# Optimization experiments

Measured on AMD Instinct MI355X. Metric: run time of the kernel, lower is better.

## Reference

```python
import jax, jax.numpy as jnp
import numpy as np

B, L, E, D = 4, 1024, 128, 256
NPOI, EPOI, NH, FF = 10000, 128, 8, 256
HD = D // NH


def layer_norm(x, g, b, eps=1e-5):
    m = x.mean(-1, keepdims=True)
    v = ((x - m) ** 2).mean(-1, keepdims=True)
    return (x - m) / jnp.sqrt(v + eps) * g + b


def leaky_relu(x):
    return jnp.where(x >= 0, x, 0.01 * x)


def tokenize_timestamp(t):
    # t: (..., 2) = [timestamp_sec, delta_sec] -> (..., 4) = [week, hour, minute, d_minute]
    week = t[..., 0] % 604800.0 / 86400.0
    hour = t[..., 0] % 86400.0 / 3600.0
    minute = t[..., 0] % 3600.0 / 60.0
    return jnp.stack([week, hour, minute, t[..., 1] / 60.0], -1)


def pos_encode(pos, d):
    # standard sinusoidal PE evaluated at integer positions `pos`
    freq = jnp.exp(-jnp.log(10000.0) * (2.0 * jnp.arange(d // 2, dtype=jnp.float32)) / d)
    ang = pos[..., None].astype(jnp.float32) * freq  # (..., d/2)
    pe = jnp.zeros(pos.shape + (d,), jnp.float32)
    return pe.at[..., 0::2].set(jnp.sin(ang)).at[..., 1::2].set(jnp.cos(ang))


def setup_inputs():
    ks = iter(jax.random.split(jax.random.key(0), 48))

    def nrm(shape, s=0.02):
        return jax.random.normal(next(ks), shape, jnp.float32) * s

    spatial = jax.random.normal(next(ks), (B, L, 2), jnp.float32) * 10.0
    ts = jax.random.uniform(next(ks), (B, L), jnp.float32, 0.0, 1e6)
    dt = jax.random.uniform(next(ks), (B, L), jnp.float32, 0.0, 3600.0)
    token = jax.random.randint(next(ks), (B, L, 2), 0, 2).astype(jnp.float32)
    iq = jnp.zeros((B, L, 4, 2), jnp.float32)
    iq = iq.at[..., 0, 0].set(spatial[..., 0]).at[..., 1, 0].set(spatial[..., 1])
    iq = iq.at[..., 2, 0].set(ts).at[..., 3, 0].set(dt)
    iq = iq.at[..., 0, 1].set(token[..., 0]).at[..., 2, 1].set(token[..., 1])
    positions = jax.random.randint(next(ks), (B, L, 2), 0, L)
    return dict(
        input_seq=iq, positions=positions,
        poi_coors=jax.random.normal(next(ks), (NPOI, 2), jnp.float32) * 10.0,
        poi_embed_mat=nrm((NPOI, EPOI), 1.0),
        sp_w1=nrm((2, E)), sp_b1=jnp.zeros((E,), jnp.float32),
        sp_w2=nrm((E, D)), sp_b2=jnp.zeros((D,), jnp.float32),
        four_w=nrm((4, E), 1.0), four_b=nrm((4, E), 1.0),
        te_w=nrm((4 * E, D)), te_b=jnp.zeros((D,), jnp.float32),
        poi_ln_g=jnp.ones((EPOI,), jnp.float32), poi_ln_b=jnp.zeros((EPOI,), jnp.float32),
        poi_w=nrm((EPOI, D)), poi_b=jnp.zeros((D,), jnp.float32),
        tok_emb=nrm((6, E), 1.0).at[5].set(0.0),
        tok_ln_g=jnp.ones((E,), jnp.float32), tok_ln_b=jnp.zeros((E,), jnp.float32),
        tok_w=nrm((E, D)), tok_b=jnp.zeros((D,), jnp.float32),
        mha_in_w=nrm((D, 3 * D)), mha_in_b=jnp.zeros((3 * D,), jnp.float32),
        mha_out_w=nrm((D, D)), mha_out_b=jnp.zeros((D,), jnp.float32),
        ln1_g=jnp.ones((D,), jnp.float32), ln1_b=jnp.zeros((D,), jnp.float32),
        ff_w1=nrm((D, FF)), ff_b1=jnp.zeros((FF,), jnp.float32),
        ff_w2=nrm((FF, D)), ff_b2=jnp.zeros((D,), jnp.float32),
        ln2_g=jnp.ones((D,), jnp.float32), ln2_b=jnp.zeros((D,), jnp.float32))


def reference(input_seq, positions, poi_coors, poi_embed_mat,
              sp_w1, sp_b1, sp_w2, sp_b2, four_w, four_b, te_w, te_b,
              poi_ln_g, poi_ln_b, poi_w, poi_b,
              tok_emb, tok_ln_g, tok_ln_b, tok_w, tok_b,
              mha_in_w, mha_in_b, mha_out_w, mha_out_b,
              ln1_g, ln1_b, ff_w1, ff_b1, ff_w2, ff_b2, ln2_g, ln2_b):
    token = input_seq[..., jnp.array([0, 2]), 1].astype(jnp.int32)  # (B,L,2)
    spatial = input_seq[:, :, 0:2, 0]                                # (B,L,2)
    tt = tokenize_timestamp(input_seq[:, :, 2:4, 0])                 # (B,L,4)
    # token embedding: Embedding(6) -> LN -> Linear -> (B,L,2,D)
    tok_e = layer_norm(tok_emb[token], tok_ln_g, tok_ln_b) @ tok_w + tok_b
    # spatial embedding (note: original's masked_fill is non-inplace and discarded)
    sp_e = leaky_relu(spatial @ sp_w1 + sp_b1) @ sp_w2 + sp_b2 + tok_e[:, :, 0]
    # brute-force nearest POI: cdist^2 + argmin + gather
    d2 = ((poi_coors[None, None] - spatial[:, :, None]) ** 2).sum(-1)  # (B,L,NPOI)
    poi = jnp.argmin(d2, -1)                                           # (B,L)
    poi_e = layer_norm(poi_embed_mat[poi], poi_ln_g, poi_ln_b) @ poi_w + poi_b + tok_e[:, :, 0]
    # temporal: 4 FourierEncode modules -> concat -> LeakyReLU -> Linear
    t_e = jnp.cos(tt[..., None] * four_w + four_b).reshape(B, L, 4 * E)
    t_e = leaky_relu(t_e) @ te_w + te_b + tok_e[:, :, 1]
    # modal mixer: 1-layer post-norm TransformerEncoder over the 3 modalities
    x = jnp.stack([sp_e, t_e, poi_e], 2).reshape(B * L, 3, D)
    qkv = x @ mha_in_w + mha_in_b
    q, k, v = jnp.split(qkv, 3, -1)
    q = q.reshape(B * L, 3, NH, HD)
    k = k.reshape(B * L, 3, NH, HD)
    v = v.reshape(B * L, 3, NH, HD)
    att = jax.nn.softmax(jnp.einsum('nqhd,nkhd->nhqk', q, k) / jnp.sqrt(jnp.float32(HD)), -1)
    o = jnp.einsum('nhqk,nkhd->nqhd', att, v).reshape(B * L, 3, D) @ mha_out_w + mha_out_b
    x = layer_norm(x + o, ln1_g, ln1_b)
    x = layer_norm(x + (jax.nn.relu(x @ ff_w1 + ff_b1) @ ff_w2 + ff_b2), ln2_g, ln2_b)
    modal_h = x.reshape(B, L, 3, D).mean(2)
    modal_h = modal_h + pos_encode(positions[..., 0], D) + pos_encode(positions[..., 1], D)
    return modal_h  # == mem_seq in the original forward
```

## Files before the change

### kernel.cpp

```cpp
#include <hip/hip_runtime.h>
#include <math.h>

namespace {
constexpr int E = 128, D = 256;
constexpr int NPOI = 10000, NH = 8, FFD = 256;
constexpr int HD = D / NH;
constexpr int NTOK = 4096;
constexpr int TA = 4;
constexpr int TB = 4;
constexpr float LN_EPS = 1e-5f;

constexpr int PK_QKV = 0;
constexpr int PK_OUT = 196608;
constexpr int PK_FF1 = 262144;
constexpr int PK_FF2 = 327680;
constexpr int PK_E0  = 393216;
constexpr int PK_E1  = 458752;
constexpr int PK_E2  = 622592;
constexpr int PK_TOTAL = 688128;
}

using frag8 = __attribute__((ext_vector_type(8))) short;
using f32x4 = __attribute__((ext_vector_type(4))) float;

__device__ __forceinline__ float bf2f(short s) {
    union { unsigned u; float f; } x; x.u = ((unsigned)(unsigned short)s) << 16; return x.f;
}
__device__ __forceinline__ unsigned short f2bf(float f) {
    union { float f; unsigned u; } x; x.f = f;
    unsigned r = x.u + 0x7fffu + ((x.u >> 16) & 1u);
    return (unsigned short)(r >> 16);
}

__device__ __forceinline__ float wsum64(float v) {
#pragma unroll
    for (int m = 1; m < 64; m <<= 1) v += __shfl_xor(v, m);
    return v;
}

__device__ __forceinline__ void ln128_bf(const float* __restrict__ src,
                                         const float* __restrict__ g,
                                         const float* __restrict__ b,
                                         short* __restrict__ dst1,
                                         short* __restrict__ dst2, int lane) {
    float v0 = src[lane], v1 = src[64 + lane];
    float mean = wsum64(v0 + v1) * (1.0f / 128.0f);
    float d0 = v0 - mean, d1 = v1 - mean;
    float var = wsum64(d0 * d0 + d1 * d1) * (1.0f / 128.0f);
    float inv = sqrtf(var + LN_EPS);
    float y0 = d0 / inv * g[lane] + b[lane];
    float y1 = d1 / inv * g[64 + lane] + b[64 + lane];
    unsigned short s0 = f2bf(y0), s1 = f2bf(y1);
    dst1[lane] = (short)s0; dst1[64 + lane] = (short)s1;
    if (dst2) { dst2[lane] = (short)s0; dst2[64 + lane] = (short)s1; }
}

__global__ __launch_bounds__(256)
void pack_weights(const float* __restrict__ wqkv, const float* __restrict__ wout,
                  const float* __restrict__ fw1,  const float* __restrict__ fw2,
                  const float* __restrict__ sp_w2, const float* __restrict__ te_w,
                  const float* __restrict__ poi_w, const float* __restrict__ tok_w,
                  unsigned short* __restrict__ pk)
{
    int idx = blockIdx.x * 256 + threadIdx.x;
    if (idx >= PK_TOTAL) return;
    int base, NKT, sel;
    if (idx < PK_OUT)      { base = PK_QKV; NKT = 8;  sel = 0; }
    else if (idx < PK_FF1) { base = PK_OUT; NKT = 8;  sel = 1; }
    else if (idx < PK_FF2) { base = PK_FF1; NKT = 8;  sel = 2; }
    else if (idx < PK_E0)  { base = PK_FF2; NKT = 8;  sel = 3; }
    else if (idx < PK_E1)  { base = PK_E0;  NKT = 8;  sel = 4; }
    else if (idx < PK_E2)  { base = PK_E1;  NKT = 20; sel = 5; }
    else                   { base = PK_E2;  NKT = 8;  sel = 6; }
    int loc = idx - base;
    int j = loc & 7, l = (loc >> 3) & 63, t = loc >> 9;
    int kt = t % NKT, nt = t / NKT;
    int k = kt * 32 + (l >> 4) * 8 + j;
    int n = nt * 16 + (l & 15);
    float v;
    switch (sel) {
        case 0: v = wqkv[(size_t)k * 768 + n]; break;
        case 1: v = wout[(size_t)k * 256 + n]; break;
        case 2: v = fw1[(size_t)k * 256 + n]; break;
        case 3: v = fw2[(size_t)k * 256 + n]; break;
        case 4: v = (k < 128) ? sp_w2[(size_t)k * 256 + n] : tok_w[(size_t)(k - 128) * 256 + n]; break;
        case 5: v = (k < 512) ? te_w[(size_t)k * 256 + n]  : tok_w[(size_t)(k - 512) * 256 + n]; break;
        default: v = (k < 128) ? poi_w[(size_t)k * 256 + n] : tok_w[(size_t)(k - 128) * 256 + n]; break;
    }
    pk[idx] = f2bf(v);
}

__global__ __launch_bounds__(256, 4)
void embed_mfma(const float* __restrict__ iq,
                const float* __restrict__ poi_coors,
                const float* __restrict__ poi_embed,
                const float* __restrict__ sp_w1, const float* __restrict__ sp_b1,
                const float* __restrict__ sp_b2,
                const float* __restrict__ four_w, const float* __restrict__ four_b,
                const float* __restrict__ te_b,
                const float* __restrict__ poi_ln_g, const float* __restrict__ poi_ln_b,
                const float* __restrict__ poi_b,
                const float* __restrict__ tok_emb,
                const float* __restrict__ tok_ln_g, const float* __restrict__ tok_ln_b,
                const float* __restrict__ tok_b,
                const unsigned short* __restrict__ pk,
                float* __restrict__ xout)
{
    constexpr int P0 = 264, P1 = 648, P2 = 264;
    const int tid = threadIdx.x;
    const int w = tid >> 6, lane = tid & 63;
    const int quad = lane >> 4, l16 = lane & 15;
    const int n0 = blockIdx.x * TA;

    __shared__ __align__(16) short s_h0[16 * P0];
    __shared__ __align__(16) short s_h1[16 * P1];
    __shared__ __align__(16) short s_h2[16 * P2];
    __shared__ float s_meta[TA][6];
    __shared__ int   s_tok[TA][2];
    __shared__ float s_wd[4][TA];
    __shared__ int   s_wi[4][TA];
    __shared__ int   s_poi[TA];

    if (tid < TA) {
        const float* p = iq + (size_t)(n0 + tid) * 8;
        s_meta[tid][0] = p[0];
        s_meta[tid][1] = p[2];
        float ts = p[4];
        float dt = p[6];
        s_tok[tid][0] = (int)p[1];
        s_tok[tid][1] = (int)p[5];
        s_meta[tid][2] = fmodf(ts, 604800.0f) / 86400.0f;
        s_meta[tid][3] = fmodf(ts, 86400.0f) / 3600.0f;
        s_meta[tid][4] = fmodf(ts, 3600.0f) / 60.0f;
        s_meta[tid][5] = dt / 60.0f;
    }
    __syncthreads();

    {
        float sx[TA], sy[TA], bd[TA];
        int bi[TA];
#pragma unroll
        for (int t = 0; t < TA; ++t) {
            sx[t] = s_meta[t][0]; sy[t] = s_meta[t][1];
            bd[t] = INFINITY; bi[t] = NPOI;
        }
        const float2* pc = (const float2*)poi_coors;
        for (int i = tid; i < NPOI; i += 256) {
            float2 p = pc[i];
#pragma unroll
            for (int t = 0; t < TA; ++t) {
                float dx = __fsub_rn(p.x, sx[t]);
                float dy = __fsub_rn(p.y, sy[t]);
                float d  = __fadd_rn(__fmul_rn(dx, dx), __fmul_rn(dy, dy));
                if (d < bd[t]) { bd[t] = d; bi[t] = i; }
            }
        }
#pragma unroll
        for (int m = 1; m < 64; m <<= 1) {
#pragma unroll
            for (int t = 0; t < TA; ++t) {
                float od = __shfl_xor(bd[t], m);
                int   oi = __shfl_xor(bi[t], m);
                if (od < bd[t] || (od == bd[t] && oi < bi[t])) { bd[t] = od; bi[t] = oi; }
            }
        }
        if (lane == 0) {
#pragma unroll
            for (int t = 0; t < TA; ++t) { s_wd[w][t] = bd[t]; s_wi[w][t] = bi[t]; }
        }
        __syncthreads();
        if (tid < TA) {
            float bdd = s_wd[0][tid]; int bii = s_wi[0][tid];
#pragma unroll
            for (int ww = 1; ww < 4; ++ww) {
                float od = s_wd[ww][tid]; int oi = s_wi[ww][tid];
                if (od < bdd || (od == bdd && oi < bii)) { bdd = od; bii = oi; }
            }
            s_poi[tid] = bii;
        }
        __syncthreads();
    }

    {
        const int t = w;
        ln128_bf(tok_emb + (size_t)s_tok[t][0] * E, tok_ln_g, tok_ln_b,
                 s_h0 + t * P0 + 128, s_h2 + t * P2 + 128, lane);
        ln128_bf(tok_emb + (size_t)s_tok[t][1] * E, tok_ln_g, tok_ln_b,
                 s_h1 + t * P1 + 512, nullptr, lane);
        ln128_bf(poi_embed + (size_t)s_poi[t] * E, poi_ln_g, poi_ln_b,
                 s_h2 + t * P2, nullptr, lane);
    }

    for (int idx = tid; idx < TA * 128; idx += 256) {
        int t = idx >> 7, l = idx & 127;
        float h = s_meta[t][0] * sp_w1[l] + s_meta[t][1] * sp_w1[128 + l] + sp_b1[l];
        s_h0[t * P0 + l] = (short)f2bf((h >= 0.0f) ? h : 0.01f * h);
    }
    for (int idx = tid; idx < TA * 512; idx += 256) {
        int t = idx >> 9, jj = idx & 511, f = jj >> 7;
        float c = cosf(s_meta[t][2 + f] * four_w[jj] + four_b[jj]);
        s_h1[t * P1 + jj] = (short)f2bf((c >= 0.0f) ? c : 0.01f * c);
    }
    __syncthreads();

    {
        f32x4 acc[4];
#pragma unroll
        for (int nt = 0; nt < 4; ++nt) {
            int c = w * 64 + nt * 16 + l16;
            float bv = sp_b2[c] + tok_b[c];
            acc[nt][0] = bv; acc[nt][1] = bv; acc[nt][2] = bv; acc[nt][3] = bv;
        }
        for (int kt = 0; kt < 8; ++kt) {
            frag8 a = *(const frag8*)(&s_h0[l16 * P0 + kt * 32 + quad * 8]);
#pragma unroll
            for (int nt = 0; nt < 4; ++nt) {
                frag8 b = *(const frag8*)(pk + PK_E0 + (((size_t)(w * 4 + nt) * 8 + kt) * 64 + lane) * 8);
                acc[nt] = __builtin_amdgcn_mfma_f32_16x16x32_bf16(a, b, acc[nt], 0, 0, 0);
            }
        }
        if (quad == 0) {
#pragma unroll
            for (int nt = 0; nt < 4; ++nt)
#pragma unroll
                for (int r = 0; r < 4; ++r)
                    xout[(size_t)(n0 + r) * 768 + w * 64 + nt * 16 + l16] = acc[nt][r];
        }
    }
    {
        f32x4 acc[4];
#pragma unroll
        for (int nt = 0; nt < 4; ++nt) {
            int c = w * 64 + nt * 16 + l16;
            float bv = te_b[c] + tok_b[c];
            acc[nt][0] = bv; acc[nt][1] = bv; acc[nt][2] = bv; acc[nt][3] = bv;
        }
        for (int kt = 0; kt < 20; ++kt) {
            frag8 a = *(const frag8*)(&s_h1[l16 * P1 + kt * 32 + quad * 8]);
#pragma unroll
            for (int nt = 0; nt < 4; ++nt) {
                frag8 b = *(const frag8*)(pk + PK_E1 + (((size_t)(w * 4 + nt) * 20 + kt) * 64 + lane) * 8);
                acc[nt] = __builtin_amdgcn_mfma_f32_16x16x32_bf16(a, b, acc[nt], 0, 0, 0);
            }
        }
        if (quad == 0) {
#pragma unroll
            for (int nt = 0; nt < 4; ++nt)
#pragma unroll
                for (int r = 0; r < 4; ++r)
                    xout[(size_t)(n0 + r) * 768 + 256 + w * 64 + nt * 16 + l16] = acc[nt][r];
        }
    }
    {
        f32x4 acc[4];
#pragma unroll
        for (int nt = 0; nt < 4; ++nt) {
            int c = w * 64 + nt * 16 + l16;
            float bv = poi_b[c] + tok_b[c];
            acc[nt][0] = bv; acc[nt][1] = bv; acc[nt][2] = bv; acc[nt][3] = bv;
        }
        for (int kt = 0; kt < 8; ++kt) {
            frag8 a = *(const frag8*)(&s_h2[l16 * P2 + kt * 32 + quad * 8]);
#pragma unroll
            for (int nt = 0; nt < 4; ++nt) {
                frag8 b = *(const frag8*)(pk + PK_E2 + (((size_t)(w * 4 + nt) * 8 + kt) * 64 + lane) * 8);
                acc[nt] = __builtin_amdgcn_mfma_f32_16x16x32_bf16(a, b, acc[nt], 0, 0, 0);
            }
        }
        if (quad == 0) {
#pragma unroll
            for (int nt = 0; nt < 4; ++nt)
#pragma unroll
                for (int r = 0; r < 4; ++r)
                    xout[(size_t)(n0 + r) * 768 + 512 + w * 64 + nt * 16 + l16] = acc[nt][r];
        }
    }
}

__global__ __launch_bounds__(256, 4)
void mha_ff_mfma(const float* __restrict__ xin,
                 const unsigned short* __restrict__ pk,
                 const float* __restrict__ bqkv, const float* __restrict__ bout,
                 const float* __restrict__ ln1g, const float* __restrict__ ln1b,
                 const float* __restrict__ fb1,  const float* __restrict__ fb2,
                 const float* __restrict__ ln2g, const float* __restrict__ ln2b,
                 const int* __restrict__ positions,
                 float* __restrict__ out)
{
    constexpr int PA = 264;
    constexpr int PQ = 776;
    constexpr int PF = 260;
    constexpr int NROW = 3 * TB;
    const int tid = threadIdx.x;
    const int w = tid >> 6, lane = tid & 63;
    const int quad = lane >> 4, l16 = lane & 15;
    const int n0tok = blockIdx.x * TB;
    const float* xg = xin + (size_t)n0tok * 3 * D;

    __shared__ __align__(16) short s_a[16 * PA];
    __shared__ __align__(16) char  s_u[25088];
    __shared__ float s_att[TB * NH * 9];

    short* s_qkv = (short*)s_u;
    float* s_f   = (float*)s_u;
    short* s_h   = (short*)(s_u + 16 * PF * 4);

    for (int i = tid * 4; i < NROW * 256; i += 1024) {
        float4 v = *(const float4*)(xg + i);
        int row = i >> 8, col = i & 255;
        ushort4 bb;
        bb.x = f2bf(v.x); bb.y = f2bf(v.y); bb.z = f2bf(v.z); bb.w = f2bf(v.w);
        *(ushort4*)(&s_a[row * PA + col]) = bb;
    }
    __syncthreads();

    {
        f32x4 acc[12];
#pragma unroll
        for (int nt = 0; nt < 12; ++nt) {
            float bv = bqkv[w * 192 + nt * 16 + l16];
            acc[nt][0] = bv; acc[nt][1] = bv; acc[nt][2] = bv; acc[nt][3] = bv;
        }
        for (int kt = 0; kt < 8; ++kt) {
            frag8 a = *(const frag8*)(&s_a[l16 * PA + kt * 32 + quad * 8]);
#pragma unroll
            for (int nt = 0; nt < 12; ++nt) {
                frag8 b = *(const frag8*)(pk + PK_QKV + (((size_t)(w * 12 + nt) * 8 + kt) * 64 + lane) * 8);
                acc[nt] = __builtin_amdgcn_mfma_f32_16x16x32_bf16(a, b, acc[nt], 0, 0, 0);
            }
        }
#pragma unroll
        for (int nt = 0; nt < 12; ++nt)
#pragma unroll
            for (int r = 0; r < 4; ++r) {
                int row = quad * 4 + r, col = w * 192 + nt * 16 + l16;
                s_qkv[row * PQ + col] = (short)f2bf(acc[nt][r]);
            }
    }
    __syncthreads();

    for (int idx = tid; idx < TB * NH * 9; idx += 256) {
        int tok = idx / 72, rem = idx % 72;
        int h = rem / 9, qr = (rem % 9) / 3, kr = rem % 3;
        const short* qp = s_qkv + (tok * 3 + qr) * PQ + h * HD;
        const short* kp = s_qkv + (tok * 3 + kr) * PQ + D + h * HD;
        float s = 0.0f;
#pragma unroll
        for (int u = 0; u < HD; ++u) s += bf2f(qp[u]) * bf2f(kp[u]);
        s_att[idx] = s / sqrtf((float)HD);
    }
    __syncthreads();
    for (int idx3 = tid; idx3 < TB * NH * 3; idx3 += 256) {
        float* a = s_att + idx3 * 3;
        float m = fmaxf(a[0], fmaxf(a[1], a[2]));
        float e0 = expf(a[0] - m), e1 = expf(a[1] - m), e2 = expf(a[2] - m);
        float inv = 1.0f / (e0 + e1 + e2);
        a[0] = e0 * inv; a[1] = e1 * inv; a[2] = e2 * inv;
    }
    __syncthreads();

    {
        const int h = tid >> 5;
#pragma unroll
        for (int tok = 0; tok < TB; ++tok) {
            float v0 = bf2f(s_qkv[(tok * 3 + 0) * PQ + 2 * D + tid]);
            float v1 = bf2f(s_qkv[(tok * 3 + 1) * PQ + 2 * D + tid]);
            float v2 = bf2f(s_qkv[(tok * 3 + 2) * PQ + 2 * D + tid]);
#pragma unroll
            for (int qr = 0; qr < 3; ++qr) {
                const float* a = s_att + tok * 72 + h * 9 + qr * 3;
                s_a[(tok * 3 + qr) * PA + tid] = (short)f2bf(a[0] * v0 + a[1] * v1 + a[2] * v2);
            }
        }
    }
    __syncthreads();

    {
        f32x4 acc[4];
#pragma unroll
        for (int nt = 0; nt < 4; ++nt) {
            float bv = bout[w * 64 + nt * 16 + l16];
            acc[nt][0] = bv; acc[nt][1] = bv; acc[nt][2] = bv; acc[nt][3] = bv;
        }
        for (int kt = 0; kt < 8; ++kt) {
            frag8 a = *(const frag8*)(&s_a[l16 * PA + kt * 32 + quad * 8]);
#pragma unroll
            for (int nt = 0; nt < 4; ++nt) {
                frag8 b = *(const frag8*)(pk + PK_OUT + (((size_t)(w * 4 + nt) * 8 + kt) * 64 + lane) * 8);
                acc[nt] = __builtin_amdgcn_mfma_f32_16x16x32_bf16(a, b, acc[nt], 0, 0, 0);
            }
        }
#pragma unroll
        for (int nt = 0; nt < 4; ++nt)
#pragma unroll
            for (int r = 0; r < 4; ++r) {
                int row = quad * 4 + r, col = w * 64 + nt * 16 + l16;
                float xr = (row < NROW) ? xg[row * 256 + col] : 0.0f;
                s_f[row * PF + col] = acc[nt][r] + xr;
            }
    }
    __syncthreads();

#pragma unroll
    for (int rr = 0; rr < 4; ++rr) {
        int row = w + rr * 4, col = lane * 4;
        float4 v = *(const float4*)(&s_f[row * PF + col]);
        float mean = wsum64(v.x + v.y + v.z + v.w) * (1.0f / 256.0f);
        float dx = v.x - mean, dy = v.y - mean, dz = v.z - mean, dw = v.w - mean;
        float var = wsum64(dx * dx + dy * dy + dz * dz + dw * dw) * (1.0f / 256.0f);
        float s = sqrtf(var + LN_EPS);
        float4 g = *(const float4*)(ln1g + col), b = *(const float4*)(ln1b + col);
        float y0 = dx / s * g.x + b.x, y1 = dy / s * g.y + b.y;
        float y2 = dz / s * g.z + b.z, y3 = dw / s * g.w + b.w;
        float4 yv; yv.x = y0; yv.y = y1; yv.z = y2; yv.w = y3;
        *(float4*)(&s_f[row * PF + col]) = yv;
        ushort4 bb; bb.x = f2bf(y0); bb.y = f2bf(y1); bb.z = f2bf(y2); bb.w = f2bf(y3);
        *(ushort4*)(&s_a[row * PA + col]) = bb;
    }
    __syncthreads();

    {
        f32x4 acc[4];
#pragma unroll
        for (int nt = 0; nt < 4; ++nt) {
            float bv = fb1[w * 64 + nt * 16 + l16];
            acc[nt][0] = bv; acc[nt][1] = bv; acc[nt][2] = bv; acc[nt][3] = bv;
        }
        for (int kt = 0; kt < 8; ++kt) {
            frag8 a = *(const frag8*)(&s_a[l16 * PA + kt * 32 + quad * 8]);
#pragma unroll
            for (int nt = 0; nt < 4; ++nt) {
                frag8 b = *(const frag8*)(pk + PK_FF1 + (((size_t)(w * 4 + nt) * 8 + kt) * 64 + lane) * 8);
                acc[nt] = __builtin_amdgcn_mfma_f32_16x16x32_bf16(a, b, acc[nt], 0, 0, 0);
            }
        }
#pragma unroll
        for (int nt = 0; nt < 4; ++nt)
#pragma unroll
            for (int r = 0; r < 4; ++r) {
                int row = quad * 4 + r, col = w * 64 + nt * 16 + l16;
                s_h[row * PA + col] = (short)f2bf(fmaxf(acc[nt][r], 0.0f));
            }
    }
    __syncthreads();

    {
        f32x4 acc[4];
#pragma unroll
        for (int nt = 0; nt < 4; ++nt) {
            float bv = fb2[w * 64 + nt * 16 + l16];
            acc[nt][0] = bv; acc[nt][1] = bv; acc[nt][2] = bv; acc[nt][3] = bv;
        }
        for (int kt = 0; kt < 8; ++kt) {
            frag8 a = *(const frag8*)(&s_h[l16 * PA + kt * 32 + quad * 8]);
#pragma unroll
            for (int nt = 0; nt < 4; ++nt) {
                frag8 b = *(const frag8*)(pk + PK_FF2 + (((size_t)(w * 4 + nt) * 8 + kt) * 64 + lane) * 8);
                acc[nt] = __builtin_amdgcn_mfma_f32_16x16x32_bf16(a, b, acc[nt], 0, 0, 0);
            }
        }
#pragma unroll
        for (int nt = 0; nt < 4; ++nt)
#pragma unroll
            for (int r = 0; r < 4; ++r) {
                int row = quad * 4 + r, col = w * 64 + nt * 16 + l16;
                float y = s_f[row * PF + col];
                s_f[row * PF + col] = acc[nt][r] + y;
            }
    }
    __syncthreads();

#pragma unroll
    for (int rr = 0; rr < 4; ++rr) {
        int row = w + rr * 4, col = lane * 4;
        float4 v = *(const float4*)(&s_f[row * PF + col]);
        float mean = wsum64(v.x + v.y + v.z + v.w) * (1.0f / 256.0f);
        float dx = v.x - mean, dy = v.y - mean, dz = v.z - mean, dw = v.w - mean;
        float var = wsum64(dx * dx + dy * dy + dz * dz + dw * dw) * (1.0f / 256.0f);
        float s = sqrtf(var + LN_EPS);
        float4 g = *(const float4*)(ln2g + col), b = *(const float4*)(ln2b + col);
        float4 zv;
        zv.x = dx / s * g.x + b.x; zv.y = dy / s * g.y + b.y;
        zv.z = dz / s * g.z + b.z; zv.w = dw / s * g.w + b.w;
        *(float4*)(&s_f[row * PF + col]) = zv;
    }
    __syncthreads();

    {
        const int fi = tid >> 1;
        const float freq = expf(-logf(10000.0f) * (2.0f * fi) / (float)D);
#pragma unroll
        for (int t = 0; t < TB; ++t) {
            int n = n0tok + t;
            float m3 = (s_f[(3 * t) * PF + tid] + s_f[(3 * t + 1) * PF + tid] +
                        s_f[(3 * t + 2) * PF + tid]) / 3.0f;
            float p0 = (float)positions[2 * n], p1 = (float)positions[2 * n + 1];
            float a0 = p0 * freq, a1 = p1 * freq;
            float pe = (tid & 1) ? (cosf(a0) + cosf(a1)) : (sinf(a0) + sinf(a1));
            out[(size_t)n * D + tid] = m3 + pe;
        }
    }
}

extern "C" void kernel_launch(void* const* d_in, const int* in_sizes, int n_in,
                              void* d_out, int out_size, void* d_ws, size_t ws_size,
                              hipStream_t stream)
{
    const float* iq        = (const float*)d_in[0];
    const int*   positions = (const int*)d_in[1];
    const float* poi_coors = (const float*)d_in[2];
    const float* poi_embed = (const float*)d_in[3];
    const float* sp_w1     = (const float*)d_in[4];
    const float* sp_b1     = (const float*)d_in[5];
    const float* sp_w2     = (const float*)d_in[6];
    const float* sp_b2     = (const float*)d_in[7];
    const float* four_w    = (const float*)d_in[8];
    const float* four_b    = (const float*)d_in[9];
    const float* te_w      = (const float*)d_in[10];
    const float* te_b      = (const float*)d_in[11];
    const float* poi_ln_g  = (const float*)d_in[12];
    const float* poi_ln_b  = (const float*)d_in[13];
    const float* poi_w     = (const float*)d_in[14];
    const float* poi_b     = (const float*)d_in[15];
    const float* tok_emb   = (const float*)d_in[16];
    const float* tok_ln_g  = (const float*)d_in[17];
    const float* tok_ln_b  = (const float*)d_in[18];
    const float* tok_w     = (const float*)d_in[19];
    const float* tok_b     = (const float*)d_in[20];
    const float* mha_in_w  = (const float*)d_in[21];
    const float* mha_in_b  = (const float*)d_in[22];
    const float* mha_out_w = (const float*)d_in[23];
    const float* mha_out_b = (const float*)d_in[24];
    const float* ln1_g     = (const float*)d_in[25];
    const float* ln1_b     = (const float*)d_in[26];
    const float* ff_w1     = (const float*)d_in[27];
    const float* ff_b1     = (const float*)d_in[28];
    const float* ff_w2     = (const float*)d_in[29];
    const float* ff_b2     = (const float*)d_in[30];
    const float* ln2_g     = (const float*)d_in[31];
    const float* ln2_b     = (const float*)d_in[32];

    float* xws = (float*)d_ws;
    unsigned short* pkw = (unsigned short*)((char*)d_ws + (size_t)NTOK * 3 * D * 4);

    pack_weights<<<(PK_TOTAL + 255) / 256, 256, 0, stream>>>(
        mha_in_w, mha_out_w, ff_w1, ff_w2, sp_w2, te_w, poi_w, tok_w, pkw);

    embed_mfma<<<NTOK / TA, 256, 0, stream>>>(
        iq, poi_coors, poi_embed, sp_w1, sp_b1, sp_b2, four_w, four_b,
        te_b, poi_ln_g, poi_ln_b, poi_b, tok_emb, tok_ln_g, tok_ln_b, tok_b,
        pkw, xws);

    mha_ff_mfma<<<NTOK / TB, 256, 0, stream>>>(
        xws, pkw, mha_in_b, mha_out_b, ln1_g, ln1_b,
        ff_b1, ff_b2, ln2_g, ln2_b, positions, (float*)d_out);
}
```

Baseline: 221.8 us.

## Fuse embedding and mixer kernels and tile weight packing through LDS

Merges the embedding kernel and the MHA/FFN kernel into one fused kernel. The three modality embeddings now go straight into LDS as bf16 instead of a round trip through fp32 global workspace, with the LDS regions reused across stages. The weight packing kernel is also rewritten: each wave loads a 32x16 tile with float4 reads, transposes it through shared memory and writes whole 8-element fragments, replacing scattered per-element gathers. The cost is more LDS per block and a lower occupancy hint (3 instead of 4). The residual now comes from the bf16-rounded embedding rather than the fp32 one.

```diff
diff --git a/kernel.cpp b/kernel.cpp
--- a/kernel.cpp
+++ b/kernel.cpp
@@ -7,7 +7,6 @@
 constexpr int HD = D / NH;
 constexpr int NTOK = 4096;
 constexpr int TA = 4;
-constexpr int TB = 4;
 constexpr float LN_EPS = 1e-5f;
 
 constexpr int PK_QKV = 0;
@@ -18,6 +17,7 @@
 constexpr int PK_E1  = 458752;
 constexpr int PK_E2  = 622592;
 constexpr int PK_TOTAL = 688128;
+constexpr int NTILES = PK_TOTAL / 512;
 }
 
 using frag8 = __attribute__((ext_vector_type(8))) short;
@@ -62,64 +62,95 @@
                   const float* __restrict__ poi_w, const float* __restrict__ tok_w,
                   unsigned short* __restrict__ pk)
 {
-    int idx = blockIdx.x * 256 + threadIdx.x;
-    if (idx >= PK_TOTAL) return;
-    int base, NKT, sel;
-    if (idx < PK_OUT)      { base = PK_QKV; NKT = 8;  sel = 0; }
-    else if (idx < PK_FF1) { base = PK_OUT; NKT = 8;  sel = 1; }
-    else if (idx < PK_FF2) { base = PK_FF1; NKT = 8;  sel = 2; }
-    else if (idx < PK_E0)  { base = PK_FF2; NKT = 8;  sel = 3; }
-    else if (idx < PK_E1)  { base = PK_E0;  NKT = 8;  sel = 4; }
-    else if (idx < PK_E2)  { base = PK_E1;  NKT = 20; sel = 5; }
-    else                   { base = PK_E2;  NKT = 8;  sel = 6; }
-    int loc = idx - base;
-    int j = loc & 7, l = (loc >> 3) & 63, t = loc >> 9;
-    int kt = t % NKT, nt = t / NKT;
-    int k = kt * 32 + (l >> 4) * 8 + j;
-    int n = nt * 16 + (l & 15);
-    float v;
+    __shared__ float buf[4][32 * 17];
+    const int wv = threadIdx.x >> 6, lane = threadIdx.x & 63;
+    const int tile = blockIdx.x * 4 + wv;
+    if (tile >= NTILES) return;
+
+    int t = tile, sel, base;
+    if (t < 384)              { sel = 0; base = PK_QKV; }
+    else if ((t -= 384) < 128){ sel = 1; base = PK_OUT; }
+    else if ((t -= 128) < 128){ sel = 2; base = PK_FF1; }
+    else if ((t -= 128) < 128){ sel = 3; base = PK_FF2; }
+    else if ((t -= 128) < 128){ sel = 4; base = PK_E0; }
+    else if ((t -= 128) < 320){ sel = 5; base = PK_E1; }
+    else                      { t -= 320; sel = 6; base = PK_E2; }
+    const int NKT = (sel == 5) ? 20 : 8;
+    const int nt = t / NKT, kt = t % NKT;
+
+    const int k = kt * 32 + (lane >> 1);
+    const int n0 = nt * 16 + (lane & 1) * 8;
+    const float* row;
     switch (sel) {
-        case 0: v = wqkv[(size_t)k * 768 + n]; break;
-        case 1: v = wout[(size_t)k * 256 + n]; break;
-        case 2: v = fw1[(size_t)k * 256 + n]; break;
-        case 3: v = fw2[(size_t)k * 256 + n]; break;
-        case 4: v = (k < 128) ? sp_w2[(size_t)k * 256 + n] : tok_w[(size_t)(k - 128) * 256 + n]; break;
-        case 5: v = (k < 512) ? te_w[(size_t)k * 256 + n]  : tok_w[(size_t)(k - 512) * 256 + n]; break;
-        default: v = (k < 128) ? poi_w[(size_t)k * 256 + n] : tok_w[(size_t)(k - 128) * 256 + n]; break;
-    }
-    pk[idx] = f2bf(v);
-}
-
-__global__ __launch_bounds__(256, 4)
-void embed_mfma(const float* __restrict__ iq,
-                const float* __restrict__ poi_coors,
-                const float* __restrict__ poi_embed,
-                const float* __restrict__ sp_w1, const float* __restrict__ sp_b1,
-                const float* __restrict__ sp_b2,
-                const float* __restrict__ four_w, const float* __restrict__ four_b,
-                const float* __restrict__ te_b,
-                const float* __restrict__ poi_ln_g, const float* __restrict__ poi_ln_b,
-                const float* __restrict__ poi_b,
-                const float* __restrict__ tok_emb,
-                const float* __restrict__ tok_ln_g, const float* __restrict__ tok_ln_b,
-                const float* __restrict__ tok_b,
-                const unsigned short* __restrict__ pk,
-                float* __restrict__ xout)
+        case 0:  row = wqkv + (size_t)k * 768; break;
+        case 1:  row = wout + (size_t)k * 256; break;
+        case 2:  row = fw1  + (size_t)k * 256; break;
+        case 3:  row = fw2  + (size_t)k * 256; break;
+        case 4:  row = (k < 128) ? sp_w2 + (size_t)k * 256 : tok_w + (size_t)(k - 128) * 256; break;
+        case 5:  row = (k < 512) ? te_w  + (size_t)k * 256 : tok_w + (size_t)(k - 512) * 256; break;
+        default: row = (k < 128) ? poi_w + (size_t)k * 256 : tok_w + (size_t)(k - 128) * 256; break;
+    }
+    float4 v0 = *(const float4*)(row + n0);
+    float4 v1 = *(const float4*)(row + n0 + 4);
+    float* b = buf[wv];
+    const int wb = (lane >> 1) * 17 + (lane & 1) * 8;
+    b[wb + 0] = v0.x; b[wb + 1] = v0.y; b[wb + 2] = v0.z; b[wb + 3] = v0.w;
+    b[wb + 4] = v1.x; b[wb + 5] = v1.y; b[wb + 6] = v1.z; b[wb + 7] = v1.w;
+    __syncthreads();
+
+    const int rb = (lane >> 4) * 8, c = lane & 15;
+    frag8 fr;
+#pragma unroll
+    for (int j = 0; j < 8; ++j) fr[j] = (short)f2bf(b[(rb + j) * 17 + c]);
+    *(frag8*)(pk + base + ((size_t)t * 64 + lane) * 8) = fr;
+}
+
+__global__ __launch_bounds__(256, 3)
+void trajfm_fused(const float* __restrict__ iq,
+                  const float* __restrict__ poi_coors,
+                  const float* __restrict__ poi_embed,
+                  const float* __restrict__ sp_w1, const float* __restrict__ sp_b1,
+                  const float* __restrict__ sp_b2,
+                  const float* __restrict__ four_w, const float* __restrict__ four_b,
+                  const float* __restrict__ te_b,
+                  const float* __restrict__ poi_ln_g, const float* __restrict__ poi_ln_b,
+                  const float* __restrict__ poi_b,
+                  const float* __restrict__ tok_emb,
+                  const float* __restrict__ tok_ln_g, const float* __restrict__ tok_ln_b,
+                  const float* __restrict__ tok_b,
+                  const unsigned short* __restrict__ pk,
+                  const float* __restrict__ bqkv, const float* __restrict__ bout,
+                  const float* __restrict__ ln1g, const float* __restrict__ ln1b,
+                  const float* __restrict__ fb1,  const float* __restrict__ fb2,
+                  const float* __restrict__ ln2g, const float* __restrict__ ln2b,
+                  const int* __restrict__ positions,
+                  float* __restrict__ out)
 {
     constexpr int P0 = 264, P1 = 648, P2 = 264;
+    constexpr int PA = 264;
+    constexpr int PQ = 776;
+    constexpr int PF = 260;
     const int tid = threadIdx.x;
     const int w = tid >> 6, lane = tid & 63;
     const int quad = lane >> 4, l16 = lane & 15;
     const int n0 = blockIdx.x * TA;
 
-    __shared__ __align__(16) short s_h0[16 * P0];
-    __shared__ __align__(16) short s_h1[16 * P1];
-    __shared__ __align__(16) short s_h2[16 * P2];
+    __shared__ __align__(16) short s_a[16 * PA];
+    __shared__ __align__(16) char  U[37632];
+    __shared__ float s_att[TA * NH * 9];
     __shared__ float s_meta[TA][6];
     __shared__ int   s_tok[TA][2];
     __shared__ float s_wd[4][TA];
     __shared__ int   s_wi[4][TA];
     __shared__ int   s_poi[TA];
+
+    short* h0   = (short*)U;
+    short* h1   = (short*)(U + 8448);
+    short* h2   = (short*)(U + 29184);
+    short* qkv  = (short*)U;
+    short* o_b  = (short*)(U + 24832);
+    float* s_f  = (float*)U;
+    short* s_h  = (short*)(U + 16640);
 
     if (tid < TA) {
         const float* p = iq + (size_t)(n0 + tid) * 8;
@@ -184,22 +215,22 @@
     {
         const int t = w;
         ln128_bf(tok_emb + (size_t)s_tok[t][0] * E, tok_ln_g, tok_ln_b,
-                 s_h0 + t * P0 + 128, s_h2 + t * P2 + 128, lane);
+                 h0 + t * P0 + 128, h2 + t * P2 + 128, lane);
         ln128_bf(tok_emb + (size_t)s_tok[t][1] * E, tok_ln_g, tok_ln_b,
-                 s_h1 + t * P1 + 512, nullptr, lane);
+                 h1 + t * P1 + 512, nullptr, lane);
         ln128_bf(poi_embed + (size_t)s_poi[t] * E, poi_ln_g, poi_ln_b,
-                 s_h2 + t * P2, nullptr, lane);
+                 h2 + t * P2, nullptr, lane);
     }
 
     for (int idx = tid; idx < TA * 128; idx += 256) {
         int t = idx >> 7, l = idx & 127;
         float h = s_meta[t][0] * sp_w1[l] + s_meta[t][1] * sp_w1[128 + l] + sp_b1[l];
-        s_h0[t * P0 + l] = (short)f2bf((h >= 0.0f) ? h : 0.01f * h);
+        h0[t * P0 + l] = (short)f2bf((h >= 0.0f) ? h : 0.01f * h);
     }
     for (int idx = tid; idx < TA * 512; idx += 256) {
         int t = idx >> 9, jj = idx & 511, f = jj >> 7;
         float c = cosf(s_meta[t][2 + f] * four_w[jj] + four_b[jj]);
-        s_h1[t * P1 + jj] = (short)f2bf((c >= 0.0f) ? c : 0.01f * c);
+        h1[t * P1 + jj] = (short)f2bf((c >= 0.0f) ? c : 0.01f * c);
     }
     __syncthreads();
 
@@ -212,7 +243,7 @@
             acc[nt][0] = bv; acc[nt][1] = bv; acc[nt][2] = bv; acc[nt][3] = bv;
         }
         for (int kt = 0; kt < 8; ++kt) {
-            frag8 a = *(const frag8*)(&s_h0[l16 * P0 + kt * 32 + quad * 8]);
+            frag8 a = *(const frag8*)(&h0[l16 * P0 + kt * 32 + quad * 8]);
 #pragma unroll
             for (int nt = 0; nt < 4; ++nt) {
                 frag8 b = *(const frag8*)(pk + PK_E0 + (((size_t)(w * 4 + nt) * 8 + kt) * 64 + lane) * 8);
@@ -224,7 +255,7 @@
             for (int nt = 0; nt < 4; ++nt)
 #pragma unroll
                 for (int r = 0; r < 4; ++r)
-                    xout[(size_t)(n0 + r) * 768 + w * 64 + nt * 16 + l16] = acc[nt][r];
+                    s_a[(3 * r + 0) * PA + w * 64 + nt * 16 + l16] = (short)f2bf(acc[nt][r]);
         }
     }
     {
@@ -236,7 +267,7 @@
             acc[nt][0] = bv; acc[nt][1] = bv; acc[nt][2] = bv; acc[nt][3] = bv;
         }
         for (int kt = 0; kt < 20; ++kt) {
-            frag8 a = *(const frag8*)(&s_h1[l16 * P1 + kt * 32 + quad * 8]);
+            frag8 a = *(const frag8*)(&h1[l16 * P1 + kt * 32 + quad * 8]);
 #pragma unroll
             for (int nt = 0; nt < 4; ++nt) {
                 frag8 b = *(const frag8*)(pk + PK_E1 + (((size_t)(w * 4 + nt) * 20 + kt) * 64 + lane) * 8);
@@ -248,7 +279,7 @@
             for (int nt = 0; nt < 4; ++nt)
 #pragma unroll
                 for (int r = 0; r < 4; ++r)
-                    xout[(size_t)(n0 + r) * 768 + 256 + w * 64 + nt * 16 + l16] = acc[nt][r];
+                    s_a[(3 * r + 1) * PA + w * 64 + nt * 16 + l16] = (short)f2bf(acc[nt][r]);
         }
     }
     {
@@ -260,7 +291,7 @@
             acc[nt][0] = bv; acc[nt][1] = bv; acc[nt][2] = bv; acc[nt][3] = bv;
         }
         for (int kt = 0; kt < 8; ++kt) {
-            frag8 a = *(const frag8*)(&s_h2[l16 * P2 + kt * 32 + quad * 8]);
+            frag8 a = *(const frag8*)(&h2[l16 * P2 + kt * 32 + quad * 8]);
 #pragma unroll
             for (int nt = 0; nt < 4; ++nt) {
                 frag8 b = *(const frag8*)(pk + PK_E2 + (((size_t)(w * 4 + nt) * 8 + kt) * 64 + lane) * 8);
@@ -272,45 +303,8 @@
             for (int nt = 0; nt < 4; ++nt)
 #pragma unroll
                 for (int r = 0; r < 4; ++r)
-                    xout[(size_t)(n0 + r) * 768 + 512 + w * 64 + nt * 16 + l16] = acc[nt][r];
-        }
-    }
-}
-
-__global__ __launch_bounds__(256, 4)
-void mha_ff_mfma(const float* __restrict__ xin,
-                 const unsigned short* __restrict__ pk,
-                 const float* __restrict__ bqkv, const float* __restrict__ bout,
-                 const float* __restrict__ ln1g, const float* __restrict__ ln1b,
-                 const float* __restrict__ fb1,  const float* __restrict__ fb2,
-                 const float* __restrict__ ln2g, const float* __restrict__ ln2b,
-                 const int* __restrict__ positions,
-                 float* __restrict__ out)
-{
-    constexpr int PA = 264;
-    constexpr int PQ = 776;
-    constexpr int PF = 260;
-    constexpr int NROW = 3 * TB;
-    const int tid = threadIdx.x;
-    const int w = tid >> 6, lane = tid & 63;
-    const int quad = lane >> 4, l16 = lane & 15;
-    const int n0tok = blockIdx.x * TB;
-    const float* xg = xin + (size_t)n0tok * 3 * D;
-
-    __shared__ __align__(16) short s_a[16 * PA];
-    __shared__ __align__(16) char  s_u[25088];
-    __shared__ float s_att[TB * NH * 9];
-
-    short* s_qkv = (short*)s_u;
-    float* s_f   = (float*)s_u;
-    short* s_h   = (short*)(s_u + 16 * PF * 4);
-
-    for (int i = tid * 4; i < NROW * 256; i += 1024) {
-        float4 v = *(const float4*)(xg + i);
-        int row = i >> 8, col = i & 255;
-        ushort4 bb;
-        bb.x = f2bf(v.x); bb.y = f2bf(v.y); bb.z = f2bf(v.z); bb.w = f2bf(v.w);
-        *(ushort4*)(&s_a[row * PA + col]) = bb;
+                    s_a[(3 * r + 2) * PA + w * 64 + nt * 16 + l16] = (short)f2bf(acc[nt][r]);
+        }
     }
     __syncthreads();
 
@@ -334,23 +328,23 @@
 #pragma unroll
             for (int r = 0; r < 4; ++r) {
                 int row = quad * 4 + r, col = w * 192 + nt * 16 + l16;
-                s_qkv[row * PQ + col] = (short)f2bf(acc[nt][r]);
-            }
-    }
-    __syncthreads();
-
-    for (int idx = tid; idx < TB * NH * 9; idx += 256) {
+                qkv[row * PQ + col] = (short)f2bf(acc[nt][r]);
+            }
+    }
+    __syncthreads();
+
+    for (int idx = tid; idx < TA * NH * 9; idx += 256) {
         int tok = idx / 72, rem = idx % 72;
         int h = rem / 9, qr = (rem % 9) / 3, kr = rem % 3;
-        const short* qp = s_qkv + (tok * 3 + qr) * PQ + h * HD;
-        const short* kp = s_qkv + (tok * 3 + kr) * PQ + D + h * HD;
+        const short* qp = qkv + (tok * 3 + qr) * PQ + h * HD;
+        const short* kp = qkv + (tok * 3 + kr) * PQ + D + h * HD;
         float s = 0.0f;
 #pragma unroll
         for (int u = 0; u < HD; ++u) s += bf2f(qp[u]) * bf2f(kp[u]);
         s_att[idx] = s / sqrtf((float)HD);
     }
     __syncthreads();
-    for (int idx3 = tid; idx3 < TB * NH * 3; idx3 += 256) {
+    for (int idx3 = tid; idx3 < TA * NH * 3; idx3 += 256) {
         float* a = s_att + idx3 * 3;
         float m = fmaxf(a[0], fmaxf(a[1], a[2]));
         float e0 = expf(a[0] - m), e1 = expf(a[1] - m), e2 = expf(a[2] - m);
@@ -362,14 +356,14 @@
     {
         const int h = tid >> 5;
 #pragma unroll
-        for (int tok = 0; tok < TB; ++tok) {
-            float v0 = bf2f(s_qkv[(tok * 3 + 0) * PQ + 2 * D + tid]);
-            float v1 = bf2f(s_qkv[(tok * 3 + 1) * PQ + 2 * D + tid]);
-            float v2 = bf2f(s_qkv[(tok * 3 + 2) * PQ + 2 * D + tid]);
+        for (int tok = 0; tok < TA; ++tok) {
+            float v0 = bf2f(qkv[(tok * 3 + 0) * PQ + 2 * D + tid]);
+            float v1 = bf2f(qkv[(tok * 3 + 1) * PQ + 2 * D + tid]);
+            float v2 = bf2f(qkv[(tok * 3 + 2) * PQ + 2 * D + tid]);
 #pragma unroll
             for (int qr = 0; qr < 3; ++qr) {
                 const float* a = s_att + tok * 72 + h * 9 + qr * 3;
-                s_a[(tok * 3 + qr) * PA + tid] = (short)f2bf(a[0] * v0 + a[1] * v1 + a[2] * v2);
+                o_b[(tok * 3 + qr) * PA + tid] = (short)f2bf(a[0] * v0 + a[1] * v1 + a[2] * v2);
             }
         }
     }
@@ -383,7 +377,7 @@
             acc[nt][0] = bv; acc[nt][1] = bv; acc[nt][2] = bv; acc[nt][3] = bv;
         }
         for (int kt = 0; kt < 8; ++kt) {
-            frag8 a = *(const frag8*)(&s_a[l16 * PA + kt * 32 + quad * 8]);
+            frag8 a = *(const frag8*)(&o_b[l16 * PA + kt * 32 + quad * 8]);
 #pragma unroll
             for (int nt = 0; nt < 4; ++nt) {
                 frag8 b = *(const frag8*)(pk + PK_OUT + (((size_t)(w * 4 + nt) * 8 + kt) * 64 + lane) * 8);
@@ -395,8 +389,7 @@
 #pragma unroll
             for (int r = 0; r < 4; ++r) {
                 int row = quad * 4 + r, col = w * 64 + nt * 16 + l16;
-                float xr = (row < NROW) ? xg[row * 256 + col] : 0.0f;
-                s_f[row * PF + col] = acc[nt][r] + xr;
+                s_f[row * PF + col] = acc[nt][r] + bf2f(s_a[row * PA + col]);
             }
     }
     __syncthreads();
@@ -490,8 +483,8 @@
         const int fi = tid >> 1;
         const float freq = expf(-logf(10000.0f) * (2.0f * fi) / (float)D);
 #pragma unroll
-        for (int t = 0; t < TB; ++t) {
-            int n = n0tok + t;
+        for (int t = 0; t < TA; ++t) {
+            int n = n0 + t;
             float m3 = (s_f[(3 * t) * PF + tid] + s_f[(3 * t + 1) * PF + tid] +
                         s_f[(3 * t + 2) * PF + tid]) / 3.0f;
             float p0 = (float)positions[2 * n], p1 = (float)positions[2 * n + 1];
@@ -540,18 +533,14 @@
     const float* ln2_g     = (const float*)d_in[31];
     const float* ln2_b     = (const float*)d_in[32];
 
-    float* xws = (float*)d_ws;
-    unsigned short* pkw = (unsigned short*)((char*)d_ws + (size_t)NTOK * 3 * D * 4);
-
-    pack_weights<<<(PK_TOTAL + 255) / 256, 256, 0, stream>>>(
+    unsigned short* pkw = (unsigned short*)d_ws;
+
+    pack_weights<<<NTILES / 4, 256, 0, stream>>>(
         mha_in_w, mha_out_w, ff_w1, ff_w2, sp_w2, te_w, poi_w, tok_w, pkw);
 
-    embed_mfma<<<NTOK / TA, 256, 0, stream>>>(
-        iq, poi_coors, poi_embed, sp_w1, sp_b1, sp_b2, four_w, four_b,
-        te_b, poi_ln_g, poi_ln_b, poi_b, tok_emb, tok_ln_g, tok_ln_b, tok_b,
-        pkw, xws);
-
-    mha_ff_mfma<<<NTOK / TB, 256, 0, stream>>>(
-        xws, pkw, mha_in_b, mha_out_b, ln1_g, ln1_b,
-        ff_b1, ff_b2, ln2_g, ln2_b, positions, (float*)d_out);
-}
+    trajfm_fused<<<NTOK / TA, 256, 0, stream>>>(
+        iq, poi_coors, poi_embed, sp_w1, sp_b1, sp_b2, four_w, four_b, te_b,
+        poi_ln_g, poi_ln_b, poi_b, tok_emb, tok_ln_g, tok_ln_b, tok_b,
+        pkw, mha_in_b, mha_out_b, ln1_g, ln1_b, ff_b1, ff_b2, ln2_g, ln2_b,
+        positions, (float*)d_out);
+}
```

Measured after the change: 242.5 us. 1.09x slower.
